# Kernel optimization log

Measured on AMD Instinct MI355X. Metric: run time of the kernel, lower is better.

The kernel has to match this reference:

```python
import jax, jax.numpy as jnp
import numpy as np

EPS = 1e-5
KH = KW = 3
PAD = 1

def conv3x3(x, w, b=None):
    out = jax.lax.conv_general_dilated(
        x, w, window_strides=(1, 1), padding=((PAD, PAD), (PAD, PAD)),
        dimension_numbers=("NCHW", "OIHW", "NCHW"))
    if b is not None:
        out = out + b[None, :, None, None]
    return out

def batchnorm(x, gamma, beta):
    # training-mode BatchNorm2d: batch statistics over (N, H, W)
    mean = x.mean(axis=(0, 2, 3), keepdims=True)
    var = x.var(axis=(0, 2, 3), keepdims=True)
    return gamma[None, :, None, None] * (x - mean) / jnp.sqrt(var + EPS) + beta[None, :, None, None]

def bilinear_gather(x, y_pos, x_pos):
    # x: [B,C,H,W]; y_pos/x_pos: [B,P,H,W] (P = KH*KW sampling taps)
    # zero padding outside image (mmcv modulated deform conv semantics)
    B, C, H, W = x.shape
    P = y_pos.shape[1]
    x_flat = x.reshape(B, C, H * W)
    y0 = jnp.floor(y_pos)
    x0 = jnp.floor(x_pos)
    ly = y_pos - y0
    lx = x_pos - x0
    out = jnp.zeros((B, C, P, H, W), dtype=x.dtype)
    for dy, dx, wgt in ((0, 0, (1 - ly) * (1 - lx)), (0, 1, (1 - ly) * lx),
                        (1, 0, ly * (1 - lx)), (1, 1, ly * lx)):
        yi = y0 + dy
        xi = x0 + dx
        valid = ((yi >= 0) & (yi <= H - 1) & (xi >= 0) & (xi <= W - 1)).astype(x.dtype)
        yc = jnp.clip(yi, 0, H - 1).astype(jnp.int32)
        xc = jnp.clip(xi, 0, W - 1).astype(jnp.int32)
        idx = (yc * W + xc).reshape(B, 1, P * H * W)
        vals = jnp.take_along_axis(x_flat, jnp.broadcast_to(idx, (B, C, P * H * W)), axis=2)
        vals = vals.reshape(B, C, P, H, W)
        out = out + vals * (wgt * valid)[:, None]
    return out  # [B,C,P,H,W]

def modulated_deform_conv(x, w_off, b_off, w_dcn):
    B, C, H, W = x.shape
    P = KH * KW
    off = conv3x3(x, w_off, b_off)  # [B, 3*P, H, W]
    o1, o2, m = jnp.split(off, 3, axis=1)
    offset = jnp.concatenate([o1, o2], axis=1)            # [B, 2P, H, W]
    offset = offset.reshape(B, P, 2, H, W)                # channel 2p -> dy, 2p+1 -> dx
    mask = jax.nn.sigmoid(m)                              # [B, P, H, W]
    hh = jnp.arange(H, dtype=x.dtype)
    ww = jnp.arange(W, dtype=x.dtype)
    ky = jnp.arange(KH, dtype=x.dtype)
    kx = jnp.arange(KW, dtype=x.dtype)
    # base sampling grid per tap p = ky*KW + kx: (h - PAD + ky, w - PAD + kx)
    base_y = (hh[None, :] - PAD + ky[:, None])            # [KH, H]
    base_x = (ww[None, :] - PAD + kx[:, None])            # [KW, W]
    base_y = jnp.broadcast_to(base_y[:, None, :, None], (KH, KW, H, W)).reshape(P, H, W)
    base_x = jnp.broadcast_to(base_x[None, :, None, :], (KH, KW, H, W)).reshape(P, H, W)
    y_pos = base_y[None] + offset[:, :, 0]                # [B,P,H,W]
    x_pos = base_x[None] + offset[:, :, 1]
    sampled = bilinear_gather(x, y_pos, x_pos)            # [B,C,P,H,W]
    sampled = sampled * mask[:, None]
    w = w_dcn.reshape(w_dcn.shape[0], C, P)               # [O, C, P]
    return jnp.einsum("bcphw,ocp->bohw", sampled, w)

def setup_inputs() -> dict:
    key = jax.random.key(0)
    ks = jax.random.split(key, 10)
    B, Ch, H, W = 4, 256, 64, 64
    Cin, Cout = 2 * Ch, 256
    P = KH * KW
    inp = {
        "input_v": jax.random.normal(ks[0], (B, Ch, H, W), jnp.float32),
        "input_i": jax.random.normal(ks[1], (B, Ch, H, W), jnp.float32),
        "w_off": jax.random.normal(ks[2], (3 * P, Cin, KH, KW), jnp.float32) * 0.01,
        "b_off": jnp.zeros((3 * P,), jnp.float32),
        "w_dcn": jax.random.normal(ks[3], (Cout, Cin, KH, KW), jnp.float32) * (1.0 / np.sqrt(Cin * P)),
        "gamma1": jnp.ones((Cout,), jnp.float32),
        "beta1": jnp.zeros((Cout,), jnp.float32),
        "w2": jax.random.normal(ks[4], (Cout, Cout, KH, KW), jnp.float32) * (1.0 / np.sqrt(Cout * P)),
        "gamma2": jnp.ones((Cout,), jnp.float32),
        "beta2": jnp.zeros((Cout,), jnp.float32),
    }
    return inp

def reference(input_v, input_i, w_off, b_off, w_dcn, gamma1, beta1, w2, gamma2, beta2):
    x = jnp.concatenate([input_v, input_i], axis=1)
    out = modulated_deform_conv(x, w_off, b_off, w_dcn)
    out = jax.nn.relu(batchnorm(out, gamma1, beta1))
    out = jax.nn.relu(batchnorm(conv3x3(out, w2), gamma2, beta2))
    return out
```

## Files before the change

kernel.cpp:

```cpp
#include <hip/hip_runtime.h>
#include <cstdint>
#include <cstddef>

typedef unsigned short u16;
typedef __attribute__((ext_vector_type(8))) short s16x8;
typedef __attribute__((ext_vector_type(4))) float f32x4;

#define DEV __device__ __forceinline__

DEV float bf2f(short u){
  union { unsigned int i; float f; } v;
  v.i = ((unsigned int)(u16)u) << 16;
  return v.f;
}
DEV short f2bf(float f){
  union { float f; unsigned int i; } v; v.f = f;
  unsigned int u = v.i;
  u += 0x7fffu + ((u >> 16) & 1u);
  return (short)(u >> 16);
}
DEV f32x4 f32x4_zero(){
  f32x4 z;
#pragma unroll
  for(int j=0;j<4;j++) z[j]=0.f;
  return z;
}
DEV f32x4 mfma16(s16x8 a, s16x8 b, f32x4 c){
  return __builtin_amdgcn_mfma_f32_16x16x32_bf16(a, b, c, 0, 0, 0);
}
DEV void bar_lds(){
  asm volatile("s_waitcnt lgkmcnt(0)" ::: "memory");
  __builtin_amdgcn_s_barrier();
}
DEV void gload16(const u16* g, u16* l){
  __builtin_amdgcn_global_load_lds(
      (const __attribute__((address_space(1))) unsigned int*)g,
      (__attribute__((address_space(3))) unsigned int*)l, 16, 0, 0);
}

static constexpr size_t STATS_B     = 0;
static constexpr size_t OUT2_ACC_B  = 4096;
static constexpr size_t XN_PAD_B    = 16781312;
static constexpr size_t OUT1N_PAD_B = 34738176;
static constexpr size_t ZERO_BYTES  = 43659264;
static constexpr size_t OUT1_ACC_B  = 43659264;
static constexpr size_t PPIX_B      = 60436480;
static constexpr size_t PWGT_B      = 62795776;
static constexpr size_t Y_B         = 65155072;
static constexpr size_t WALL_B      = 159428608;
static constexpr size_t W2T_B       = 162181120;

__global__ void k_x_to_nhwc(const float* __restrict__ v, const float* __restrict__ vi,
                            u16* __restrict__ xn){
  __shared__ float tile[64][65];
  const int b = blockIdx.z, c0 = blockIdx.y*64, hw0 = blockIdx.x*64;
  const int h = hw0 >> 6;
  const float* src = (c0 < 256) ? (v  + ((size_t)b*256 + c0)      *4096)
                                : (vi + ((size_t)b*256 + (c0-256))*4096);
  const int t = threadIdx.x;
#pragma unroll
  for(int k=0;k<16;k++){
    int idx = t + k*256;
    int cl = idx >> 6, wl = idx & 63;
    tile[cl][wl] = src[(size_t)cl*4096 + hw0 + wl];
  }
  __syncthreads();
#pragma unroll
  for(int k=0;k<16;k++){
    int idx = t + k*256;
    int wl = idx >> 6, cl = idx & 63;
    xn[((size_t)(b*66 + h+1)*66 + wl+1)*512 + c0 + cl] = (u16)f2bf(tile[cl][wl]);
  }
}

__global__ void k_prep_wall(const float* __restrict__ wdcn, const float* __restrict__ woff,
                            u16* __restrict__ wt){
  int idx = blockIdx.x*256 + threadIdx.x;
  if(idx >= 2688*512) return;
  int n = idx >> 9, c = idx & 511;
  float val = 0.f;
  if(n < 2304){
    int p = n >> 8, o = n & 255;
    val = wdcn[(size_t)(o*512 + c)*9 + p];
  } else if(n < 2592){
    int q = n - 2304, p = q >> 5, nn = q & 31;
    if(nn < 27) val = woff[(size_t)(nn*512 + c)*9 + p];
  }
  wt[idx] = (u16)f2bf(val);
}
__global__ void k_prep_w2(const float* __restrict__ w, u16* __restrict__ wt){
  int idx = blockIdx.x*256 + threadIdx.x;
  if(idx >= 256*2304) return;
  int n = idx / 2304, k = idx % 2304;
  int t = k >> 8, c = k & 255;
  wt[idx] = (u16)f2bf(w[(size_t)(n*256 + c)*9 + t]);
}

__global__ __launch_bounds__(256, 2) void k_gemm_big(
    const u16* __restrict__ A, const u16* __restrict__ wt, u16* __restrict__ Y){
  const int bid = blockIdx.x;
  const int xcd = bid & 7;
  const int j   = bid >> 3;
  const int mt  = xcd + 8*(j/21);
  const int nt  = j % 21;
  if(mt >= 137) return;
  __shared__ short A_lds[2][8][128][8];
  __shared__ short B_lds[2][8][128][8];
  const int tid = threadIdx.x;
  const int lane = tid & 63, wid = tid >> 6;
  const int quad = lane >> 4, ln = lane & 15;
  const int wm = wid >> 1, wn = wid & 1;
  const int m0 = mt * 128;
  const int n0 = nt * 128;
  constexpr int NPH = 8;
  f32x4 acc[4][4];
#pragma unroll
  for(int mf=0;mf<4;mf++)
#pragma unroll
    for(int nf=0;nf<4;nf++) acc[mf][nf] = f32x4_zero();

  auto stage = [&](int t, int bi){
    const int k0 = t*64;
#pragma unroll
    for(int i=0;i<4;i++){
      const int idx = wid*4 + i;
      const int s = idx >> 1, rh = (idx & 1)*64;
      gload16(A  + (size_t)(m0 + rh + lane)*512 + k0 + s*8, (u16*)&A_lds[bi][s][rh][0]);
      gload16(wt + (size_t)(n0 + rh + lane)*512 + k0 + s*8, (u16*)&B_lds[bi][s][rh][0]);
    }
  };
  auto compute = [&](int bi){
#pragma unroll
    for(int kk=0;kk<2;kk++){
      s16x8 af[4], bf[4];
#pragma unroll
      for(int mf=0;mf<4;mf++)
        af[mf] = *(const s16x8*)&A_lds[bi][kk*4+quad][wm*64 + mf*16 + ln][0];
#pragma unroll
      for(int nf=0;nf<4;nf++)
        bf[nf] = *(const s16x8*)&B_lds[bi][kk*4+quad][wn*64 + nf*16 + ln][0];
#pragma unroll
      for(int mf=0;mf<4;mf++)
#pragma unroll
        for(int nf=0;nf<4;nf++)
          acc[mf][nf] = mfma16(af[mf], bf[nf], acc[mf][nf]);
    }
  };

  stage(0, 0);
  asm volatile("s_waitcnt vmcnt(0)" ::: "memory");
  __builtin_amdgcn_s_barrier();
  stage(1, 1);
  for(int t = 0; t < NPH; ++t){
    const int bi = t & 1;
    compute(bi);
    bar_lds();
    if(t + 2 < NPH){
      stage(t + 2, bi);
      asm volatile("s_waitcnt vmcnt(8)" ::: "memory");
    } else {
      asm volatile("s_waitcnt vmcnt(0)" ::: "memory");
    }
    __builtin_amdgcn_sched_barrier(0);
    __builtin_amdgcn_s_barrier();
  }

#pragma unroll
  for(int mf=0;mf<4;mf++)
#pragma unroll
    for(int nf=0;nf<4;nf++){
      const int col = n0 + wn*64 + nf*16 + ln;
#pragma unroll
      for(int i=0;i<4;i++){
        const int row = m0 + wm*64 + mf*16 + quad*4 + i;
        Y[(size_t)row*2688 + col] = (u16)f2bf(acc[mf][nf][i]);
      }
    }
}

__global__ __launch_bounds__(256) void k_off_combine(
    const u16* __restrict__ Y, const float* __restrict__ boff,
    int* __restrict__ ppix, float* __restrict__ pwgt){
  __shared__ float offs[64][32];
  const int t = threadIdx.x;
  const int b = blockIdx.x >> 6, h = blockIdx.x & 63;
  const int w = t >> 2, g = t & 3;
  float acc[8];
#pragma unroll
  for(int j=0;j<8;j++) acc[j] = 0.f;
  for(int p=0;p<9;p++){
    const int pp = (b*66 + h + p/3)*66 + (w + p%3);
    s16x8 v = *(const s16x8*)(Y + (size_t)pp*2688 + 2304 + p*32 + g*8);
#pragma unroll
    for(int j=0;j<8;j++) acc[j] += bf2f(v[j]);
  }
#pragma unroll
  for(int j=0;j<8;j++) offs[w][g*8 + j] = acc[j];
  __syncthreads();
  for(int id = t; id < 576; id += 256){
    const int tp = id / 64, ww = id & 63;
    const int m = (b<<12) + (h<<6) + ww;
    float dy = offs[ww][2*tp]   + boff[2*tp];
    float dx = offs[ww][2*tp+1] + boff[2*tp+1];
    float mz = offs[ww][18+tp]  + boff[18+tp];
    float mk = 1.f / (1.f + expf(-mz));
    float ypos = (float)(h - 1 + tp/3) + dy;
    float xpos = (float)(ww - 1 + tp%3) + dx;
    float y0f = floorf(ypos), x0f = floorf(xpos);
    float ly = ypos - y0f, lx = xpos - x0f;
    int y0 = (int)y0f, x0 = (int)x0f;
    const int id4 = (m*9 + tp)*4;
#pragma unroll
    for(int k=0;k<4;k++){
      int ddy = k >> 1, ddx = k & 1;
      int yi = y0 + ddy, xi = x0 + ddx;
      int yc = yi < -1 ? -1 : (yi > 64 ? 64 : yi);
      int xc = xi < -1 ? -1 : (xi > 64 ? 64 : xi);
      float wk = (ddy ? ly : 1.f-ly) * (ddx ? lx : 1.f-lx) * mk;
      ppix[id4+k] = (b*66 + yc+1)*66 + xc+1;
      pwgt[id4+k] = wk;
    }
  }
}

__global__ __launch_bounds__(512) void k_combine(
    const u16* __restrict__ Y, const int* __restrict__ ppix,
    const float* __restrict__ pwgt, float* __restrict__ out1){
  __shared__ int   s_pp[64][9][4];
  __shared__ float s_wg[64][9][4];
  const int t = threadIdx.x;
  const int b = blockIdx.x >> 6, h = blockIdx.x & 63;
  const int m_row = (b<<12) + (h<<6);
  for(int id = t; id < 576; id += 512){
    const int mo = id / 9, tp = id - mo*9;
    const size_t i4 = ((size_t)(m_row + mo)*9 + tp)*4;
    int4   pp4 = *(const int4*)  (ppix + i4);
    float4 wg4 = *(const float4*)(pwgt + i4);
    s_pp[mo][tp][0] = pp4.x; s_pp[mo][tp][1] = pp4.y;
    s_pp[mo][tp][2] = pp4.z; s_pp[mo][tp][3] = pp4.w;
    s_wg[mo][tp][0] = wg4.x; s_wg[mo][tp][1] = wg4.y;
    s_wg[mo][tp][2] = wg4.z; s_wg[mo][tp][3] = wg4.w;
  }
  __syncthreads();
  const int wv = t >> 6, lane = t & 63;
  const int c0 = lane*4;
  const int pw0 = wv*8;
  float acc[8][4];
#pragma unroll
  for(int pw=0;pw<8;pw++)
#pragma unroll
    for(int j=0;j<4;j++) acc[pw][j] = 0.f;

  for(int tp = 0; tp < 9; ++tp){
    const int cb = tp*256 + c0;
#pragma unroll
    for(int pw=0;pw<8;pw++){
      const int px = pw0 + pw;
#pragma unroll
      for(int k=0;k<4;k++){
        const float wk = s_wg[px][tp][k];
        const int   pp = s_pp[px][tp][k];
        ushort4 v = *(const ushort4*)(Y + (size_t)pp*2688 + cb);
        acc[pw][0] = fmaf(wk, bf2f((short)v.x), acc[pw][0]);
        acc[pw][1] = fmaf(wk, bf2f((short)v.y), acc[pw][1]);
        acc[pw][2] = fmaf(wk, bf2f((short)v.z), acc[pw][2]);
        acc[pw][3] = fmaf(wk, bf2f((short)v.w), acc[pw][3]);
      }
    }
  }
#pragma unroll
  for(int pw=0;pw<8;pw++){
    float4 o4;
    o4.x = acc[pw][0]; o4.y = acc[pw][1]; o4.z = acc[pw][2]; o4.w = acc[pw][3];
    *(float4*)(out1 + (size_t)(m_row + pw0 + pw)*256 + c0) = o4;
  }
}

__global__ __launch_bounds__(256, 2) void k_gemm2(
    const u16* __restrict__ a_pad, const u16* __restrict__ wt, float* __restrict__ outa){
  const int bid = blockIdx.x;
  const int xcd = bid & 7;
  const int j   = bid >> 3;
  const int mt  = xcd + 8*(j >> 2);
  const int rest = j & 3;
  const int nt  = rest & 1;
  const int kz  = rest >> 1;
  __shared__ short A_lds[2][8][128][8];
  __shared__ short B_lds[2][8][128][8];
  const int tid = threadIdx.x;
  const int lane = tid & 63, wid = tid >> 6;
  const int quad = lane >> 4, ln = lane & 15;
  const int wm = wid >> 1, wn = wid & 1;
  const int m0 = mt * 128;
  const int n0 = nt * 128;
  const int kbase = kz * 1152;
  const int b = m0 >> 12;
  const int h0 = (m0 & 4095) >> 6;
  constexpr int NPH = 18;
  f32x4 acc[4][4];
#pragma unroll
  for(int mf=0;mf<4;mf++)
#pragma unroll
    for(int nf=0;nf<4;nf++) acc[mf][nf] = f32x4_zero();

  auto stage = [&](int t, int bi){
    const int k0 = kbase + t*64;
    const int tp = k0 >> 8, cit = k0 & 255;
    const int ty = tp/3, tx = tp - ty*3;
#pragma unroll
    for(int i=0;i<4;i++){
      const int idx = wid*4 + i;
      const int s = idx >> 1, rh = (idx & 1)*64;
      const int hh = h0 + (rh >> 6) + ty;
      gload16(a_pad + ((size_t)(b*66 + hh)*66 + lane + tx)*256 + cit + s*8,
              (u16*)&A_lds[bi][s][rh][0]);
      gload16(wt + (size_t)(n0 + rh + lane)*2304 + k0 + s*8,
              (u16*)&B_lds[bi][s][rh][0]);
    }
  };
  auto compute = [&](int bi){
#pragma unroll
    for(int kk=0;kk<2;kk++){
      s16x8 af[4], bf[4];
#pragma unroll
      for(int mf=0;mf<4;mf++)
        af[mf] = *(const s16x8*)&A_lds[bi][kk*4+quad][wm*64 + mf*16 + ln][0];
#pragma unroll
      for(int nf=0;nf<4;nf++)
        bf[nf] = *(const s16x8*)&B_lds[bi][kk*4+quad][wn*64 + nf*16 + ln][0];
#pragma unroll
      for(int mf=0;mf<4;mf++)
#pragma unroll
        for(int nf=0;nf<4;nf++)
          acc[mf][nf] = mfma16(af[mf], bf[nf], acc[mf][nf]);
    }
  };

  stage(0, 0);
  asm volatile("s_waitcnt vmcnt(0)" ::: "memory");
  __builtin_amdgcn_s_barrier();
  stage(1, 1);
  for(int t = 0; t < NPH; ++t){
    const int bi = t & 1;
    compute(bi);
    bar_lds();
    if(t + 2 < NPH){
      stage(t + 2, bi);
      asm volatile("s_waitcnt vmcnt(8)" ::: "memory");
    } else {
      asm volatile("s_waitcnt vmcnt(0)" ::: "memory");
    }
    __builtin_amdgcn_sched_barrier(0);
    __builtin_amdgcn_s_barrier();
  }

#pragma unroll
  for(int mf=0;mf<4;mf++)
#pragma unroll
    for(int nf=0;nf<4;nf++){
      const int col = n0 + wn*64 + nf*16 + ln;
#pragma unroll
      for(int i=0;i<4;i++){
        const int row = m0 + wm*64 + mf*16 + quad*4 + i;
        unsafeAtomicAdd(outa + (size_t)row*256 + col, acc[mf][nf][i]);
      }
    }
}

__global__ void k_stats(const float* __restrict__ acc, float* __restrict__ sum,
                        float* __restrict__ sq){
  const int m0 = blockIdx.x*64;
  const int c = threadIdx.x;
  float s = 0.f, q = 0.f;
  for(int i=0;i<64;i++){
    float v = acc[(size_t)(m0+i)*256 + c];
    s += v; q += v*v;
  }
  unsafeAtomicAdd(sum + c, s);
  unsafeAtomicAdd(sq + c, q);
}

__global__ void k_bn1(const float* __restrict__ acc, const float* __restrict__ sum,
                      const float* __restrict__ sq, const float* __restrict__ g,
                      const float* __restrict__ bt, u16* __restrict__ o){
  __shared__ float sc[256], sh[256];
  const int t = threadIdx.x;
  {
    float mean = sum[t] * (1.f/16384.f);
    float var  = sq[t] * (1.f/16384.f) - mean*mean;
    float rstd = rsqrtf(var + 1e-5f);
    float s = g[t] * rstd;
    sc[t] = s; sh[t] = bt[t] - mean*s;
  }
  __syncthreads();
  const int c4 = (t & 63) * 4;
  const float s0 = sc[c4], s1 = sc[c4+1], s2 = sc[c4+2], s3 = sc[c4+3];
  const float h0 = sh[c4], h1 = sh[c4+1], h2 = sh[c4+2], h3 = sh[c4+3];
#pragma unroll
  for(int k=0;k<4;k++){
    int m = blockIdx.x*16 + k*4 + (t>>6);
    int b = m >> 12, hh = (m >> 6) & 63, ww = m & 63;
    const float4 v = *(const float4*)(acc + (size_t)m*256 + c4);
    unsigned int lo = (unsigned int)(u16)f2bf(fmaxf(0.f, v.x*s0 + h0))
                    | ((unsigned int)(u16)f2bf(fmaxf(0.f, v.y*s1 + h1)) << 16);
    unsigned int hi = (unsigned int)(u16)f2bf(fmaxf(0.f, v.z*s2 + h2))
                    | ((unsigned int)(u16)f2bf(fmaxf(0.f, v.w*s3 + h3)) << 16);
    uint2 pr; pr.x = lo; pr.y = hi;
    *(uint2*)(o + ((size_t)(b*66 + hh+1)*66 + ww+1)*256 + c4) = pr;
  }
}

__global__ void k_bn2_out(const float* __restrict__ acc, const float* __restrict__ sum,
                          const float* __restrict__ sq, const float* __restrict__ g,
                          const float* __restrict__ bt, float* __restrict__ out){
  __shared__ float tile[64][65];
  __shared__ float sc[64], sh[64];
  const int t = threadIdx.x;
  const int b = blockIdx.z, c0 = blockIdx.y*64, hw0 = blockIdx.x*64;
  if(t < 64){
    int c = c0 + t;
    float mean = sum[c] * (1.f/16384.f);
    float var  = sq[c] * (1.f/16384.f) - mean*mean;
    float rstd = rsqrtf(var + 1e-5f);
    float s = g[c] * rstd;
    sc[t] = s; sh[t] = bt[c] - mean*s;
  }
  __syncthreads();
#pragma unroll
  for(int k=0;k<16;k++){
    int idx = t + k*256;
    int wl = idx >> 6, cl = idx & 63;
    float v = acc[(size_t)((b<<12) + hw0 + wl)*256 + c0 + cl];
    tile[wl][cl] = fmaxf(0.f, v*sc[cl] + sh[cl]);
  }
  __syncthreads();
#pragma unroll
  for(int k=0;k<16;k++){
    int idx = t + k*256;
    int cl = idx >> 6, wl = idx & 63;
    out[(size_t)(b*256 + c0 + cl)*4096 + hw0 + wl] = tile[wl][cl];
  }
}

extern "C" void kernel_launch(void* const* d_in, const int* in_sizes, int n_in,
                              void* d_out, int out_size, void* d_ws, size_t ws_size,
                              hipStream_t stream){
  const float* in_v  = (const float*)d_in[0];
  const float* in_i  = (const float*)d_in[1];
  const float* w_off = (const float*)d_in[2];
  const float* b_off = (const float*)d_in[3];
  const float* w_dcn = (const float*)d_in[4];
  const float* g1    = (const float*)d_in[5];
  const float* bt1   = (const float*)d_in[6];
  const float* w2    = (const float*)d_in[7];
  const float* g2    = (const float*)d_in[8];
  const float* bt2   = (const float*)d_in[9];
  float* out = (float*)d_out;
  char* ws = (char*)d_ws;

  float* stats     = (float*)(ws + STATS_B);
  float* out2_acc  = (float*)(ws + OUT2_ACC_B);
  u16*   xn_pad    = (u16*)  (ws + XN_PAD_B);
  u16*   out1n_pad = (u16*)  (ws + OUT1N_PAD_B);
  float* out1_acc  = (float*)(ws + OUT1_ACC_B);
  int*   ppix      = (int*)  (ws + PPIX_B);
  float* pwgt      = (float*)(ws + PWGT_B);
  u16*   Ymat      = (u16*)  (ws + Y_B);
  u16*   wall      = (u16*)  (ws + WALL_B);
  u16*   w2t       = (u16*)  (ws + W2T_B);
  float* sum1 = stats,       *sq1 = stats + 256;
  float* sum2 = stats + 512, *sq2 = stats + 768;

  hipMemsetAsync(ws, 0, ZERO_BYTES, stream);
  k_x_to_nhwc<<<dim3(64,8,4), 256, 0, stream>>>(in_v, in_i, xn_pad);
  k_prep_wall<<<5376, 256, 0, stream>>>(w_dcn, w_off, wall);
  k_prep_w2<<<2304, 256, 0, stream>>>(w2, w2t);
  k_gemm_big<<<3024, 256, 0, stream>>>(xn_pad, wall, Ymat);
  k_off_combine<<<256, 256, 0, stream>>>(Ymat, b_off, ppix, pwgt);
  k_combine<<<256, 512, 0, stream>>>(Ymat, ppix, pwgt, out1_acc);
  k_stats<<<256, 256, 0, stream>>>(out1_acc, sum1, sq1);
  k_bn1<<<1024, 256, 0, stream>>>(out1_acc, sum1, sq1, g1, bt1, out1n_pad);
  k_gemm2<<<512, 256, 0, stream>>>(out1n_pad, w2t, out2_acc);
  k_stats<<<256, 256, 0, stream>>>(out2_acc, sum2, sq2);
  k_bn2_out<<<dim3(64,4,4), 256, 0, stream>>>(out2_acc, sum2, sq2, g2, bt2, out);
}
```

Baseline: 359.2 us.

## Process three N-tiles per GEMM block and fuse BN1 stats into combine

The big GEMM now has each block walk three consecutive 128-wide N tiles in a single pipelined loop, flushing the accumulators at each tile boundary. This cuts the grid from 3024 to 1008 blocks and amortises the prologue and launch cost. The combine kernel also reduces per-channel sum and sum-of-squares in LDS and adds them atomically, which removes the separate k_stats pass over out1. Risks: the full vmcnt(0) wait at each boundary stalls the pipeline, fewer blocks lower occupancy and parallelism, and the float atomics make the statistics order-dependent.

After: 351.2 us, median of 2. 2.2% less time.

```diff
diff --git a/kernel.cpp b/kernel.cpp
--- a/kernel.cpp
+++ b/kernel.cpp
@@ -101,8 +101,8 @@
   const int bid = blockIdx.x;
   const int xcd = bid & 7;
   const int j   = bid >> 3;
-  const int mt  = xcd + 8*(j/21);
-  const int nt  = j % 21;
+  const int mt  = xcd + 8*(j/7);
+  const int ng  = j % 7;
   if(mt >= 137) return;
   __shared__ short A_lds[2][8][128][8];
   __shared__ short B_lds[2][8][128][8];
@@ -111,16 +111,16 @@
   const int quad = lane >> 4, ln = lane & 15;
   const int wm = wid >> 1, wn = wid & 1;
   const int m0 = mt * 128;
-  const int n0 = nt * 128;
-  constexpr int NPH = 8;
+  constexpr int NPH = 24;
   f32x4 acc[4][4];
 #pragma unroll
   for(int mf=0;mf<4;mf++)
 #pragma unroll
     for(int nf=0;nf<4;nf++) acc[mf][nf] = f32x4_zero();
 
-  auto stage = [&](int t, int bi){
-    const int k0 = t*64;
+  auto stage = [&](int p, int bi){
+    const int n0 = (ng*3 + (p >> 3)) * 128;
+    const int k0 = (p & 7) * 64;
 #pragma unroll
     for(int i=0;i<4;i++){
       const int idx = wid*4 + i;
@@ -146,36 +146,41 @@
           acc[mf][nf] = mfma16(af[mf], bf[nf], acc[mf][nf]);
     }
   };
+  auto flushY = [&](int pass){
+    const int n0 = (ng*3 + pass) * 128;
+#pragma unroll
+    for(int mf=0;mf<4;mf++)
+#pragma unroll
+      for(int nf=0;nf<4;nf++){
+        const int col = n0 + wn*64 + nf*16 + ln;
+#pragma unroll
+        for(int i=0;i<4;i++){
+          const int row = m0 + wm*64 + mf*16 + quad*4 + i;
+          Y[(size_t)row*2688 + col] = (u16)f2bf(acc[mf][nf][i]);
+        }
+        acc[mf][nf] = f32x4_zero();
+      }
+  };
 
   stage(0, 0);
   asm volatile("s_waitcnt vmcnt(0)" ::: "memory");
   __builtin_amdgcn_s_barrier();
   stage(1, 1);
-  for(int t = 0; t < NPH; ++t){
-    const int bi = t & 1;
+  for(int p = 0; p < NPH; ++p){
+    const int bi = p & 1;
     compute(bi);
     bar_lds();
-    if(t + 2 < NPH){
-      stage(t + 2, bi);
+    const bool boundary = (p & 7) == 7;
+    if(boundary) flushY(p >> 3);
+    if(p + 2 < NPH) stage(p + 2, bi);
+    if(boundary || p + 2 >= NPH){
+      asm volatile("s_waitcnt vmcnt(0)" ::: "memory");
+    } else {
       asm volatile("s_waitcnt vmcnt(8)" ::: "memory");
-    } else {
-      asm volatile("s_waitcnt vmcnt(0)" ::: "memory");
     }
     __builtin_amdgcn_sched_barrier(0);
     __builtin_amdgcn_s_barrier();
   }
-
-#pragma unroll
-  for(int mf=0;mf<4;mf++)
-#pragma unroll
-    for(int nf=0;nf<4;nf++){
-      const int col = n0 + wn*64 + nf*16 + ln;
-#pragma unroll
-      for(int i=0;i<4;i++){
-        const int row = m0 + wm*64 + mf*16 + quad*4 + i;
-        Y[(size_t)row*2688 + col] = (u16)f2bf(acc[mf][nf][i]);
-      }
-    }
 }
 
 __global__ __launch_bounds__(256) void k_off_combine(
@@ -225,9 +230,11 @@
 
 __global__ __launch_bounds__(512) void k_combine(
     const u16* __restrict__ Y, const int* __restrict__ ppix,
-    const float* __restrict__ pwgt, float* __restrict__ out1){
+    const float* __restrict__ pwgt, float* __restrict__ out1,
+    float* __restrict__ sum1, float* __restrict__ sq1){
   __shared__ int   s_pp[64][9][4];
   __shared__ float s_wg[64][9][4];
+  __shared__ float s_red[2][8][256];
   const int t = threadIdx.x;
   const int b = blockIdx.x >> 6, h = blockIdx.x & 63;
   const int m_row = (b<<12) + (h<<6);
@@ -268,11 +275,30 @@
       }
     }
   }
+  float ls[4] = {0.f,0.f,0.f,0.f}, lq[4] = {0.f,0.f,0.f,0.f};
 #pragma unroll
   for(int pw=0;pw<8;pw++){
     float4 o4;
     o4.x = acc[pw][0]; o4.y = acc[pw][1]; o4.z = acc[pw][2]; o4.w = acc[pw][3];
     *(float4*)(out1 + (size_t)(m_row + pw0 + pw)*256 + c0) = o4;
+#pragma unroll
+    for(int j=0;j<4;j++){
+      ls[j] += acc[pw][j];
+      lq[j] = fmaf(acc[pw][j], acc[pw][j], lq[j]);
+    }
+  }
+#pragma unroll
+  for(int j=0;j<4;j++){
+    s_red[0][wv][c0+j] = ls[j];
+    s_red[1][wv][c0+j] = lq[j];
+  }
+  __syncthreads();
+  if(t < 256){
+    float S = 0.f, Q = 0.f;
+#pragma unroll
+    for(int w8=0;w8<8;w8++){ S += s_red[0][w8][t]; Q += s_red[1][w8][t]; }
+    unsafeAtomicAdd(sum1 + t, S);
+    unsafeAtomicAdd(sq1 + t, Q);
   }
 }
 
@@ -475,10 +501,9 @@
   k_x_to_nhwc<<<dim3(64,8,4), 256, 0, stream>>>(in_v, in_i, xn_pad);
   k_prep_wall<<<5376, 256, 0, stream>>>(w_dcn, w_off, wall);
   k_prep_w2<<<2304, 256, 0, stream>>>(w2, w2t);
-  k_gemm_big<<<3024, 256, 0, stream>>>(xn_pad, wall, Ymat);
+  k_gemm_big<<<1008, 256, 0, stream>>>(xn_pad, wall, Ymat);
   k_off_combine<<<256, 256, 0, stream>>>(Ymat, b_off, ppix, pwgt);
-  k_combine<<<256, 512, 0, stream>>>(Ymat, ppix, pwgt, out1_acc);
-  k_stats<<<256, 256, 0, stream>>>(out1_acc, sum1, sq1);
+  k_combine<<<256, 512, 0, stream>>>(Ymat, ppix, pwgt, out1_acc, sum1, sq1);
   k_bn1<<<1024, 256, 0, stream>>>(out1_acc, sum1, sq1, g1, bt1, out1n_pad);
   k_gemm2<<<512, 256, 0, stream>>>(out1n_pad, w2t, out2_acc);
   k_stats<<<256, 256, 0, stream>>>(out2_acc, sum2, sq2);
```
